# Kernel optimization log

Hardware: AMD Instinct MI355X
Metric: run time of the kernel (lower is better)

The kernel has to match this reference:

```python
import jax, jax.numpy as jnp
import numpy as np

B, N, DIM, HEADS, DEPTH, MLP = 4, 1024, 256, 4, 4, 1024
DH = DIM // HEADS
EPS = 1e-5


def _ln(x, g, b):
    mu = jnp.mean(x, axis=-1, keepdims=True)
    var = jnp.mean((x - mu) ** 2, axis=-1, keepdims=True)
    return (x - mu) / jnp.sqrt(var + EPS) * g + b


def setup_inputs() -> dict:
    key = jax.random.key(0)
    ks = jax.random.split(key, 10)
    s = 0.02
    p = {}
    p["x"] = jax.random.normal(ks[0], (B, N, DIM), jnp.float32)
    p["attn_bias"] = jax.random.normal(ks[1], (2, B, HEADS, N, N), jnp.float32)
    p["ln1_g"] = jnp.ones((DEPTH, DIM), jnp.float32)
    p["ln1_b"] = jnp.zeros((DEPTH, DIM), jnp.float32)
    p["Wkv"] = jax.random.normal(ks[2], (DEPTH, DIM, 2 * DIM), jnp.float32) * s
    p["Wq"] = jax.random.normal(ks[3], (DEPTH, DIM, DIM), jnp.float32) * s
    p["Wo"] = jax.random.normal(ks[4], (DEPTH, DIM, DIM), jnp.float32) * s
    p["bo"] = jnp.zeros((DEPTH, DIM), jnp.float32)
    p["ln2_g"] = jnp.ones((DEPTH, DIM), jnp.float32)
    p["ln2_b"] = jnp.zeros((DEPTH, DIM), jnp.float32)
    p["W1"] = jax.random.normal(ks[5], (DEPTH, DIM, MLP), jnp.float32) * s
    p["b1"] = jnp.zeros((DEPTH, MLP), jnp.float32)
    p["W2"] = jax.random.normal(ks[6], (DEPTH, MLP, DIM), jnp.float32) * s
    p["b2"] = jnp.zeros((DEPTH, DIM), jnp.float32)
    p["Wg"] = jax.random.normal(ks[7], (DIM, DIM), jnp.float32) * s
    p["lng_g"] = jnp.ones((DIM,), jnp.float32)
    p["lng_b"] = jnp.zeros((DIM,), jnp.float32)
    return p


def reference(x, attn_bias, ln1_g, ln1_b, Wkv, Wq, Wo, bo, ln2_g, ln2_b, W1, b1, W2, b2, Wg, lng_g, lng_b):
    scale = DIM ** -0.5
    add_attn = attn_bias[0] + attn_bias[1]            # [B,H,N,N]
    # aggregation bias matrices are layer-invariant (recomputed identically each layer in torch)
    A = jnp.mean(attn_bias[0], axis=1)                # [B,N,N]
    S = jnp.mean(attn_bias[1], axis=1)
    G = jax.nn.softmax(A * S, axis=2)                 # [B,N,N]

    def split_heads(t):  # [B,N,DIM] -> [B,H,N,DH]
        return t.reshape(B, N, HEADS, DH).transpose(0, 2, 1, 3)

    for l in range(DEPTH):
        # softmax-GCN aggregation
        x_ma = jax.nn.relu(_ln(jnp.matmul(G, x) @ Wg, lng_g, lng_b))
        # attention (PreNorm on x only; q comes from un-normed x_ma)
        xn = _ln(x, ln1_g[l], ln1_b[l])
        kv = xn @ Wkv[l]
        k, v = jnp.split(kv, 2, axis=-1)
        q = x_ma @ Wq[l]
        qh, kh, vh = split_heads(q), split_heads(k), split_heads(v)
        dots = jnp.einsum('bhid,bhjd->bhij', qh, kh) * scale + add_attn
        attn = jax.nn.softmax(dots, axis=-1)
        out = jnp.einsum('bhij,bhjd->bhid', attn, vh)
        out = out.transpose(0, 2, 1, 3).reshape(B, N, DIM)
        x = x + out @ Wo[l] + bo[l]
        # feed-forward (exact GELU, matching torch nn.GELU default)
        xn2 = _ln(x, ln2_g[l], ln2_b[l])
        x = x + jax.nn.gelu(xn2 @ W1[l] + b1[l], approximate=False) @ W2[l] + b2[l]
    return x
```

## Files before the change

### kernel.cpp

```cpp
#include <hip/hip_runtime.h>
#include <hip/hip_bf16.h>
#include <math.h>

typedef unsigned short u16;
typedef __bf16 bf16x8 __attribute__((ext_vector_type(8)));
typedef float f32x4 __attribute__((ext_vector_type(4)));

#define B_ 4
#define N_ 1024
#define DIM_ 256
#define HEADS_ 4
#define DH_ 64
#define MLP_ 1024
#define DEPTH_ 4

__device__ __forceinline__ float r2f(u16 r){ return __uint_as_float(((unsigned)r)<<16); }
__device__ __forceinline__ u16 f2r(float f){ __hip_bfloat16 h = __float2bfloat16(f); return *(u16*)&h; }

__device__ __forceinline__ float gelu_exact(float v){
  return 0.5f*v*(1.0f + erff(v*0.70710678118654752440f));
}

#define MFMA16(a,b,c) __builtin_amdgcn_mfma_f32_16x16x32_bf16(a,b,c,0,0,0)

__global__ void prep_bias(const float* __restrict__ bias, u16* __restrict__ G, u16* __restrict__ bsum){
  int blk = blockIdx.x;
  int i = blk & (N_-1);
  int b = blk >> 10;
  int t = threadIdx.x;
  __shared__ float red[256];
  long long base0 = ((long long)(b*HEADS_)*N_ + i)*(long long)N_;
  const long long hs = (long long)N_*N_;
  const long long cs = (long long)B_*HEADS_*N_*N_;
  int j0 = t*4;
  f32x4 a = {0.f,0.f,0.f,0.f}, s = {0.f,0.f,0.f,0.f};
  #pragma unroll
  for (int h=0;h<HEADS_;h++){
    f32x4 x0 = *(const f32x4*)(bias + base0 + h*hs + j0);
    f32x4 x1 = *(const f32x4*)(bias + cs + base0 + h*hs + j0);
    a += x0; s += x1;
    union { ushort4 u; u16 e[4]; } pk;
    #pragma unroll
    for (int k=0;k<4;k++) pk.e[k] = f2r(x0[k]+x1[k]);
    *(ushort4*)(bsum + base0 + h*hs + j0) = pk.u;
  }
  float v[4]; float lmax = -3e38f;
  #pragma unroll
  for (int k=0;k<4;k++){ v[k] = (a[k]*0.25f)*(s[k]*0.25f); lmax = fmaxf(lmax, v[k]); }
  red[t]=lmax; __syncthreads();
  for (int st=128;st>0;st>>=1){ if(t<st) red[t]=fmaxf(red[t],red[t+st]); __syncthreads(); }
  float m = red[0]; __syncthreads();
  float e[4]; float lsum = 0.f;
  #pragma unroll
  for (int k=0;k<4;k++){ e[k] = __expf(v[k]-m); lsum += e[k]; }
  red[t]=lsum; __syncthreads();
  for (int st=128;st>0;st>>=1){ if(t<st) red[t]+=red[t+st]; __syncthreads(); }
  float inv = 1.0f/red[0];
  u16* Grow = G + ((long long)b*N_ + i)*(long long)N_;
  union { ushort4 u; u16 e[4]; } pg;
  #pragma unroll
  for (int k=0;k<4;k++) pg.e[k] = f2r(e[k]*inv);
  *(ushort4*)(Grow + j0) = pg.u;
}

__global__ void ln_kernel(const float* __restrict__ X, u16* __restrict__ Y,
                          const float* __restrict__ g, const float* __restrict__ bvec){
  int row = blockIdx.x*8 + (threadIdx.x>>5);
  int cg = threadIdx.x&31;
  const float* xp = X + (long long)row*DIM_ + cg*8;
  f32x4 v0 = *(const f32x4*)xp;
  f32x4 v1 = *(const f32x4*)(xp+4);
  float s = v0[0]+v0[1]+v0[2]+v0[3]+v1[0]+v1[1]+v1[2]+v1[3];
  s += __shfl_xor(s,1); s += __shfl_xor(s,2); s += __shfl_xor(s,4); s += __shfl_xor(s,8); s += __shfl_xor(s,16);
  float mu = s*(1.0f/256.0f);
  float s2 = 0.f;
  #pragma unroll
  for (int k=0;k<4;k++){ float d=v0[k]-mu; s2 += d*d; }
  #pragma unroll
  for (int k=0;k<4;k++){ float d=v1[k]-mu; s2 += d*d; }
  s2 += __shfl_xor(s2,1); s2 += __shfl_xor(s2,2); s2 += __shfl_xor(s2,4); s2 += __shfl_xor(s2,8); s2 += __shfl_xor(s2,16);
  float rstd = rsqrtf(s2*(1.0f/256.0f)+1e-5f);
  f32x4 g0 = *(const f32x4*)(g + cg*8);
  f32x4 g1 = *(const f32x4*)(g + cg*8 + 4);
  f32x4 b0 = *(const f32x4*)(bvec + cg*8);
  f32x4 b1 = *(const f32x4*)(bvec + cg*8 + 4);
  union { ushort4 u[2]; u16 e[8]; } pk;
  #pragma unroll
  for (int k=0;k<4;k++) pk.e[k]   = f2r((v0[k]-mu)*rstd*g0[k] + b0[k]);
  #pragma unroll
  for (int k=0;k<4;k++) pk.e[4+k] = f2r((v1[k]-mu)*rstd*g1[k] + b1[k]);
  u16* yp = Y + (long long)row*DIM_ + cg*8;
  *(ushort4*)yp = pk.u[0];
  *(ushort4*)(yp+4) = pk.u[1];
}

__global__ void tcast_all(const float* __restrict__ Wkv, const float* __restrict__ Wq,
                          const float* __restrict__ Wo, const float* __restrict__ W1,
                          const float* __restrict__ W2, const float* __restrict__ Wg,
                          const float* __restrict__ xin,
                          u16* WkvT, u16* WqT, u16* WoT, u16* W1T, u16* W2T, u16* WgT, u16* xT){
  int z = blockIdx.z;
  const float* I; u16* O; int ldin, R, C;
  if (z < 4)       { I = Wkv + z*131072;      O = WkvT + z*131072;      ldin=512;  R=256;  C=512;  }
  else if (z < 8)  { I = Wq  + (z-4)*65536;   O = WqT  + (z-4)*65536;   ldin=256;  R=256;  C=256;  }
  else if (z < 12) { I = Wo  + (z-8)*65536;   O = WoT  + (z-8)*65536;   ldin=256;  R=256;  C=256;  }
  else if (z < 16) { I = W1  + (z-12)*262144; O = W1T  + (z-12)*262144; ldin=1024; R=256;  C=1024; }
  else if (z < 20) { I = W2  + (z-16)*262144; O = W2T  + (z-16)*262144; ldin=256;  R=1024; C=256;  }
  else if (z == 20){ I = Wg;                  O = WgT;                  ldin=256;  R=256;  C=256;  }
  else             { I = xin + (z-21)*262144; O = xT   + (z-21)*262144; ldin=256;  R=1024; C=256;  }
  int c0 = blockIdx.x*32, r0 = blockIdx.y*32;
  if (c0 >= C || r0 >= R) return;
  __shared__ float tile[32][33];
  int tx = threadIdx.x, ty = threadIdx.y;
  #pragma unroll
  for (int i=0;i<4;i++)
    tile[ty*4+i][tx] = I[(long long)(r0+ty*4+i)*ldin + c0+tx];
  __syncthreads();
  #pragma unroll
  for (int i=0;i<4;i++)
    O[(long long)(c0+ty*4+i)*R + r0+tx] = f2r(tile[tx][ty*4+i]);
}

__global__ __launch_bounds__(512) void layer_pre(
    const u16* __restrict__ Gb, const u16* __restrict__ xT, const u16* __restrict__ xnb,
    const u16* __restrict__ WgT, const u16* __restrict__ WqT, const u16* __restrict__ WkvT,
    const float* __restrict__ lng, const float* __restrict__ lnb,
    u16* __restrict__ qb, u16* __restrict__ kvb, u16* __restrict__ vt)
{
  __shared__ float Gx_s[16][264];
  __shared__ float t2_s[16][264];
  __shared__ u16  xma_s[16][264];
  int tid = threadIdx.x;
  int w = tid>>6, lane = tid&63, lr = lane&15, qd = lane>>4;
  int row0 = blockIdx.x*16;
  int batch = row0>>10, brow0 = row0&1023;

  {
    int kw = w>>2, cw = w&3;
    const u16* Ap = Gb + (long long)batch*1048576 + (long long)(brow0+lr)*1024 + kw*512;
    const u16* Bp = xT + (long long)batch*262144 + (long long)kw*512;
    f32x4 acc[4] = {};
    for (int k0=0;k0<512;k0+=32){
      bf16x8 af = *(const bf16x8*)(Ap + k0 + qd*8);
      #pragma unroll
      for (int nt=0;nt<4;nt++){
        bf16x8 bf = *(const bf16x8*)(Bp + (long long)(cw*64+nt*16+lr)*1024 + k0 + qd*8);
        acc[nt] = MFMA16(af,bf,acc[nt]);
      }
    }
    if (kw==0){
      #pragma unroll
      for (int nt=0;nt<4;nt++)
        #pragma unroll
        for (int r=0;r<4;r++) Gx_s[qd*4+r][cw*64+nt*16+lr] = acc[nt][r];
    }
    __syncthreads();
    if (kw==1){
      #pragma unroll
      for (int nt=0;nt<4;nt++)
        #pragma unroll
        for (int r=0;r<4;r++) Gx_s[qd*4+r][cw*64+nt*16+lr] += acc[nt][r];
    }
    __syncthreads();
  }
  {
    int r = tid>>5, cg = tid&31;
    #pragma unroll
    for (int i=0;i<8;i++) xma_s[r][cg*8+i] = f2r(Gx_s[r][cg*8+i]);
  }
  __syncthreads();
  {
    f32x4 acc[2] = {};
    for (int k0=0;k0<256;k0+=32){
      bf16x8 af = *(const bf16x8*)&xma_s[lr][k0+qd*8];
      #pragma unroll
      for (int i=0;i<2;i++){
        bf16x8 bf = *(const bf16x8*)(WgT + (long long)((w*2+i)*16+lr)*256 + k0 + qd*8);
        acc[i] = MFMA16(af,bf,acc[i]);
      }
    }
    #pragma unroll
    for (int i=0;i<2;i++)
      #pragma unroll
      for (int r=0;r<4;r++) t2_s[qd*4+r][(w*2+i)*16+lr] = acc[i][r];
  }
  __syncthreads();
  {
    int r = tid>>5, cg = tid&31;
    float v[8]; float s=0.f;
    #pragma unroll
    for (int i=0;i<8;i++){ v[i] = t2_s[r][cg*8+i]; s += v[i]; }
    s += __shfl_xor(s,1); s += __shfl_xor(s,2); s += __shfl_xor(s,4); s += __shfl_xor(s,8); s += __shfl_xor(s,16);
    float mu = s*(1.0f/256.0f);
    float s2=0.f;
    #pragma unroll
    for (int i=0;i<8;i++){ float d=v[i]-mu; s2 += d*d; }
    s2 += __shfl_xor(s2,1); s2 += __shfl_xor(s2,2); s2 += __shfl_xor(s2,4); s2 += __shfl_xor(s2,8); s2 += __shfl_xor(s2,16);
    float rstd = rsqrtf(s2*(1.0f/256.0f)+1e-5f);
    #pragma unroll
    for (int i=0;i<8;i++){
      int c = cg*8+i;
      float y = (v[i]-mu)*rstd*lng[c] + lnb[c];
      xma_s[r][c] = f2r(fmaxf(y,0.f));
    }
  }
  __syncthreads();
  {
    f32x4 acc[2] = {};
    for (int k0=0;k0<256;k0+=32){
      bf16x8 af = *(const bf16x8*)&xma_s[lr][k0+qd*8];
      #pragma unroll
      for (int i=0;i<2;i++){
        bf16x8 bf = *(const bf16x8*)(WqT + (long long)((w*2+i)*16+lr)*256 + k0 + qd*8);
        acc[i] = MFMA16(af,bf,acc[i]);
      }
    }
    #pragma unroll
    for (int i=0;i<2;i++)
      #pragma unroll
      for (int r=0;r<4;r++)
        qb[(long long)(row0+qd*4+r)*DIM_ + (w*2+i)*16+lr] = f2r(acc[i][r]);
  }
  {
    const u16* Ap = xnb + (long long)(row0+lr)*DIM_;
    f32x4 acc[4] = {};
    for (int k0=0;k0<256;k0+=32){
      bf16x8 af = *(const bf16x8*)(Ap + k0 + qd*8);
      #pragma unroll
      for (int i=0;i<4;i++){
        bf16x8 bf = *(const bf16x8*)(WkvT + (long long)((w*4+i)*16+lr)*256 + k0 + qd*8);
        acc[i] = MFMA16(af,bf,acc[i]);
      }
    }
    #pragma unroll
    for (int i=0;i<4;i++){
      int col = (w*4+i)*16+lr;
      #pragma unroll
      for (int r=0;r<4;r++){
        int row = row0+qd*4+r;
        float v = acc[i][r];
        kvb[(long long)row*512 + col] = f2r(v);
        if (col >= 256)
          vt[(long long)batch*262144 + (long long)(col-256)*1024 + (row&1023)] = f2r(v);
      }
    }
  }
}

__global__ __launch_bounds__(512) void flash_attn(
    const u16* __restrict__ qb, const u16* __restrict__ kvb,
    const u16* __restrict__ vt, const u16* __restrict__ bsum,
    u16* __restrict__ out)
{
  int z = blockIdx.z;
  int b = z>>2, h = z&3;
  int qt = blockIdx.x;
  int tid = threadIdx.x;
  int w = tid>>6, lane = tid&63;
  int g = w>>2, tw = w&3;
  int lr = lane&15, qd = lane>>4;
  __shared__ u16 Pl[8][16][72];
  __shared__ u16 sb[8][16][72];
  __shared__ float Ol[8][16][68];
  __shared__ float Ml[8][16];
  __shared__ float Ll[8][16];

  int qrow0 = qt*64 + tw*16;
  const u16* qp = qb + ((long long)(b*N_) + qrow0 + lr)*DIM_ + h*DH_;
  bf16x8 aq0 = *(const bf16x8*)(qp + qd*8);
  bf16x8 aq1 = *(const bf16x8*)(qp + 32 + qd*8);

  f32x4 oacc[4] = {};
  float m_r[4] = {-3e38f,-3e38f,-3e38f,-3e38f};
  float l_r[4] = {0.f,0.f,0.f,0.f};

  const u16* kbase = kvb + ((long long)(b*N_))*512 + h*DH_;
  const u16* vbase = vt + (long long)b*(DIM_*N_) + (long long)(h*DH_)*N_;
  const u16* bias_base = bsum + ((long long)z*N_ + qrow0)*(long long)N_;
  int srr = lane>>2, scc = (lane&3)*16;

  for (int jtl=0; jtl<8; jtl++){
    int j0 = (g*8 + jtl)*64;
    {
      const u16* gs = bias_base + (long long)srr*N_ + j0 + scc;
      uint4 t0 = *(const uint4*)gs;
      uint4 t1 = *(const uint4*)(gs+8);
      *(uint4*)&sb[w][srr][scc]   = t0;
      *(uint4*)&sb[w][srr][scc+8] = t1;
    }
    f32x4 sacc[4] = {};
    #pragma unroll
    for (int nt=0; nt<4; nt++){
      const u16* kp = kbase + (long long)(j0 + nt*16 + lr)*512;
      bf16x8 bk0 = *(const bf16x8*)(kp + qd*8);
      bf16x8 bk1 = *(const bf16x8*)(kp + 32 + qd*8);
      sacc[nt] = MFMA16(aq0, bk0, sacc[nt]);
      sacc[nt] = MFMA16(aq1, bk1, sacc[nt]);
    }
    #pragma unroll
    for (int r=0;r<4;r++){
      float pv[4];
      float vmax = -3e38f;
      #pragma unroll
      for (int nt=0;nt<4;nt++){
        float v = sacc[nt][r]*0.0625f + r2f(sb[w][qd*4+r][nt*16+lr]);
        pv[nt] = v;
        vmax = fmaxf(vmax, v);
      }
      vmax = fmaxf(vmax, __shfl_xor(vmax,1));
      vmax = fmaxf(vmax, __shfl_xor(vmax,2));
      vmax = fmaxf(vmax, __shfl_xor(vmax,4));
      vmax = fmaxf(vmax, __shfl_xor(vmax,8));
      float newm = fmaxf(m_r[r], vmax);
      float alpha = __expf(m_r[r]-newm);
      m_r[r] = newm;
      float psum = 0.f;
      #pragma unroll
      for (int nt=0;nt<4;nt++){
        float p = __expf(pv[nt]-newm);
        psum += p;
        Pl[w][qd*4+r][nt*16+lr] = f2r(p);
      }
      psum += __shfl_xor(psum,1);
      psum += __shfl_xor(psum,2);
      psum += __shfl_xor(psum,4);
      psum += __shfl_xor(psum,8);
      l_r[r] = l_r[r]*alpha + psum;
      #pragma unroll
      for (int ot=0;ot<4;ot++) oacc[ot][r] *= alpha;
    }
    #pragma unroll
    for (int ks=0;ks<2;ks++){
      bf16x8 ap = *(const bf16x8*)&Pl[w][lr][ks*32 + qd*8];
      #pragma unroll
      for (int ot=0;ot<4;ot++){
        const u16* vp = vbase + (long long)(ot*16+lr)*N_ + j0 + ks*32 + qd*8;
        bf16x8 bv = *(const bf16x8*)vp;
        oacc[ot] = MFMA16(ap, bv, oacc[ot]);
      }
    }
  }
  #pragma unroll
  for (int r=0;r<4;r++){
    int row = qd*4+r;
    #pragma unroll
    for (int ot=0;ot<4;ot++) Ol[w][row][ot*16+lr] = oacc[ot][r];
    if (lr==0){ Ml[w][row] = m_r[r]; Ll[w][row] = l_r[r]; }
  }
  __syncthreads();
  if (w < 4){
    #pragma unroll
    for (int r=0;r<4;r++){
      int row = qd*4+r;
      float m0 = Ml[w][row], m1 = Ml[w+4][row];
      float mm = fmaxf(m0,m1);
      float e0 = __expf(m0-mm), e1 = __expf(m1-mm);
      float inv = 1.0f/(Ll[w][row]*e0 + Ll[w+4][row]*e1);
      #pragma unroll
      for (int ot=0;ot<4;ot++){
        float o = Ol[w][row][ot*16+lr]*e0 + Ol[w+4][row][ot*16+lr]*e1;
        out[((long long)(b*N_) + qrow0 + row)*DIM_ + h*DH_ + ot*16 + lr] = f2r(o*inv);
      }
    }
  }
}

__global__ __launch_bounds__(512) void layer_post(
    const u16* __restrict__ aob, const float* __restrict__ resx,
    const u16* __restrict__ WoT, const float* __restrict__ bo,
    const float* __restrict__ ln2g, const float* __restrict__ ln2b,
    const u16* __restrict__ W1T, const float* __restrict__ b1,
    const u16* __restrict__ W2T, const float* __restrict__ b2,
    float* __restrict__ xf_out,
    const float* __restrict__ ln1g_next, const float* __restrict__ ln1b_next,
    u16* __restrict__ xn_out, u16* __restrict__ xT_out)
{
  __shared__ float v_s[16][264];
  __shared__ u16  xn2_s[16][264];
  __shared__ u16  h1_s[16][1048];
  __shared__ float xnew_s[16][264];
  int tid = threadIdx.x;
  int w = tid>>6, lane = tid&63, lr = lane&15, qd = lane>>4;
  int row0 = blockIdx.x*16;
  int batch = row0>>10;

  {
    const u16* Ap = aob + (long long)(row0+lr)*DIM_;
    f32x4 acc[2] = {};
    for (int k0=0;k0<256;k0+=32){
      bf16x8 af = *(const bf16x8*)(Ap + k0 + qd*8);
      #pragma unroll
      for (int i=0;i<2;i++){
        bf16x8 bf = *(const bf16x8*)(WoT + (long long)((w*2+i)*16+lr)*256 + k0 + qd*8);
        acc[i] = MFMA16(af,bf,acc[i]);
      }
    }
    #pragma unroll
    for (int i=0;i<2;i++){
      int col = (w*2+i)*16+lr;
      #pragma unroll
      for (int r=0;r<4;r++)
        v_s[qd*4+r][col] = acc[i][r] + bo[col] + resx[(long long)(row0+qd*4+r)*DIM_ + col];
    }
  }
  __syncthreads();
  {
    int r = tid>>5, cg = tid&31;
    float v[8]; float s=0.f;
    #pragma unroll
    for (int i=0;i<8;i++){ v[i] = v_s[r][cg*8+i]; s += v[i]; }
    s += __shfl_xor(s,1); s += __shfl_xor(s,2); s += __shfl_xor(s,4); s += __shfl_xor(s,8); s += __shfl_xor(s,16);
    float mu = s*(1.0f/256.0f);
    float s2=0.f;
    #pragma unroll
    for (int i=0;i<8;i++){ float d=v[i]-mu; s2 += d*d; }
    s2 += __shfl_xor(s2,1); s2 += __shfl_xor(s2,2); s2 += __shfl_xor(s2,4); s2 += __shfl_xor(s2,8); s2 += __shfl_xor(s2,16);
    float rstd = rsqrtf(s2*(1.0f/256.0f)+1e-5f);
    #pragma unroll
    for (int i=0;i<8;i++){
      int c = cg*8+i;
      xn2_s[r][c] = f2r((v[i]-mu)*rstd*ln2g[c] + ln2b[c]);
    }
  }
  __syncthreads();
  {
    f32x4 acc[8] = {};
    for (int k0=0;k0<256;k0+=32){
      bf16x8 af = *(const bf16x8*)&xn2_s[lr][k0+qd*8];
      #pragma unroll
      for (int i=0;i<8;i++){
        bf16x8 bf = *(const bf16x8*)(W1T + (long long)((w*8+i)*16+lr)*256 + k0 + qd*8);
        acc[i] = MFMA16(af,bf,acc[i]);
      }
    }
    #pragma unroll
    for (int i=0;i<8;i++){
      int col = (w*8+i)*16+lr;
      #pragma unroll
      for (int r=0;r<4;r++)
        h1_s[qd*4+r][col] = f2r(gelu_exact(acc[i][r] + b1[col]));
    }
  }
  __syncthreads();
  {
    f32x4 acc[2] = {};
    for (int k0=0;k0<1024;k0+=32){
      bf16x8 af = *(const bf16x8*)&h1_s[lr][k0+qd*8];
      #pragma unroll
      for (int i=0;i<2;i++){
        bf16x8 bf = *(const bf16x8*)(W2T + (long long)((w*2+i)*16+lr)*1024 + k0 + qd*8);
        acc[i] = MFMA16(af,bf,acc[i]);
      }
    }
    #pragma unroll
    for (int i=0;i<2;i++){
      int col = (w*2+i)*16+lr;
      #pragma unroll
      for (int r=0;r<4;r++){
        float v = acc[i][r] + b2[col] + v_s[qd*4+r][col];
        xf_out[(long long)(row0+qd*4+r)*DIM_ + col] = v;
        xnew_s[qd*4+r][col] = v;
      }
    }
  }
  if (ln1g_next){
    __syncthreads();
    int r = tid>>5, cg = tid&31;
    float v[8]; float s=0.f;
    #pragma unroll
    for (int i=0;i<8;i++){ v[i] = xnew_s[r][cg*8+i]; s += v[i]; }
    s += __shfl_xor(s,1); s += __shfl_xor(s,2); s += __shfl_xor(s,4); s += __shfl_xor(s,8); s += __shfl_xor(s,16);
    float mu = s*(1.0f/256.0f);
    float s2=0.f;
    #pragma unroll
    for (int i=0;i<8;i++){ float d=v[i]-mu; s2 += d*d; }
    s2 += __shfl_xor(s2,1); s2 += __shfl_xor(s2,2); s2 += __shfl_xor(s2,4); s2 += __shfl_xor(s2,8); s2 += __shfl_xor(s2,16);
    float rstd = rsqrtf(s2*(1.0f/256.0f)+1e-5f);
    int grow = row0 + r;
    #pragma unroll
    for (int i=0;i<8;i++){
      int c = cg*8+i;
      xn_out[(long long)grow*DIM_ + c] = f2r((v[i]-mu)*rstd*ln1g_next[c] + ln1b_next[c]);
      xT_out[(long long)batch*262144 + (long long)c*1024 + (grow&1023)] = f2r(v[i]);
    }
  }
}

extern "C" void kernel_launch(void* const* d_in, const int* in_sizes, int n_in,
                              void* d_out, int out_size, void* d_ws, size_t ws_size,
                              hipStream_t stream){
  const float* x_in   = (const float*)d_in[0];
  const float* abias  = (const float*)d_in[1];
  const float* ln1_g  = (const float*)d_in[2];
  const float* ln1_b  = (const float*)d_in[3];
  const float* Wkv    = (const float*)d_in[4];
  const float* Wq     = (const float*)d_in[5];
  const float* Wo     = (const float*)d_in[6];
  const float* bo     = (const float*)d_in[7];
  const float* ln2_g  = (const float*)d_in[8];
  const float* ln2_b  = (const float*)d_in[9];
  const float* W1     = (const float*)d_in[10];
  const float* b1     = (const float*)d_in[11];
  const float* W2     = (const float*)d_in[12];
  const float* b2     = (const float*)d_in[13];
  const float* Wg     = (const float*)d_in[14];
  const float* lng_g  = (const float*)d_in[15];
  const float* lng_b  = (const float*)d_in[16];

  char* ws = (char*)d_ws;
  float* xf   = (float*)(ws);
  u16*  Gb    = (u16*)(ws + (4ll<<20));
  u16*  bsum  = (u16*)(ws + (12ll<<20));
  u16*  kvb   = (u16*)(ws + (44ll<<20));
  u16*  vt    = (u16*)(ws + (48ll<<20));
  u16*  xT    = (u16*)(ws + (50ll<<20));
  u16*  xnb   = (u16*)(ws + (52ll<<20));
  u16*  qb    = (u16*)(ws + (54ll<<20));
  u16*  aob   = (u16*)(ws + (56ll<<20));
  u16*  WkvT  = (u16*)(ws + (58ll<<20));
  u16*  WqT   = (u16*)(ws + (59ll<<20));
  u16*  WoT   = (u16*)(ws + (59ll<<20) + (512ll<<10));
  u16*  W1T   = (u16*)(ws + (60ll<<20));
  u16*  W2T   = (u16*)(ws + (62ll<<20));
  u16*  WgT   = (u16*)(ws + (64ll<<20));

  dim3 b256(256), b512(512);

  prep_bias<<<dim3(B_*N_), b256, 0, stream>>>(abias, Gb, bsum);
  tcast_all<<<dim3(32,32,25), dim3(32,8), 0, stream>>>(Wkv,Wq,Wo,W1,W2,Wg,x_in,
                                                       WkvT,WqT,WoT,W1T,W2T,WgT,xT);
  ln_kernel<<<dim3(512), b256, 0, stream>>>(x_in, xnb, ln1_g, ln1_b);

  for (int l=0; l<DEPTH_; l++){
    const float* resx = (l==0) ? x_in : xf;
    layer_pre<<<dim3(256), b512, 0, stream>>>(Gb, xT, xnb,
        WgT, WqT + (long long)l*65536, WkvT + (long long)l*131072,
        lng_g, lng_b, qb, kvb, vt);
    flash_attn<<<dim3(16,1,B_*HEADS_), b512, 0, stream>>>(qb, kvb, vt, bsum, aob);
    if (l < DEPTH_-1){
      layer_post<<<dim3(256), b512, 0, stream>>>(aob, resx,
          WoT + (long long)l*65536, bo + l*DIM_, ln2_g + l*DIM_, ln2_b + l*DIM_,
          W1T + (long long)l*262144, b1 + l*MLP_, W2T + (long long)l*262144, b2 + l*DIM_,
          xf, ln1_g + (l+1)*DIM_, ln1_b + (l+1)*DIM_, xnb, xT);
    } else {
      layer_post<<<dim3(256), b512, 0, stream>>>(aob, resx,
          WoT + (long long)l*65536, bo + l*DIM_, ln2_g + l*DIM_, ln2_b + l*DIM_,
          W1T + (long long)l*262144, b1 + l*MLP_, W2T + (long long)l*262144, b2 + l*DIM_,
          (float*)d_out, nullptr, nullptr, nullptr, nullptr);
    }
  }
}
```

Before: 760.9 us.

## Double waves per block in layer kernels via split-K, halve flash-attn query tile

```diff
diff --git a/kernel.cpp b/kernel.cpp
--- a/kernel.cpp
+++ b/kernel.cpp
@@ -121,7 +121,7 @@
     O[(long long)(c0+ty*4+i)*R + r0+tx] = f2r(tile[tx][ty*4+i]);
 }
 
-__global__ __launch_bounds__(512) void layer_pre(
+__global__ __launch_bounds__(1024) void layer_pre(
     const u16* __restrict__ Gb, const u16* __restrict__ xT, const u16* __restrict__ xnb,
     const u16* __restrict__ WgT, const u16* __restrict__ WqT, const u16* __restrict__ WkvT,
     const float* __restrict__ lng, const float* __restrict__ lnb,
@@ -137,10 +137,10 @@
 
   {
     int kw = w>>2, cw = w&3;
-    const u16* Ap = Gb + (long long)batch*1048576 + (long long)(brow0+lr)*1024 + kw*512;
-    const u16* Bp = xT + (long long)batch*262144 + (long long)kw*512;
+    const u16* Ap = Gb + (long long)batch*1048576 + (long long)(brow0+lr)*1024 + kw*256;
+    const u16* Bp = xT + (long long)batch*262144 + (long long)kw*256;
     f32x4 acc[4] = {};
-    for (int k0=0;k0<512;k0+=32){
+    for (int k0=0;k0<256;k0+=32){
       bf16x8 af = *(const bf16x8*)(Ap + k0 + qd*8);
       #pragma unroll
       for (int nt=0;nt<4;nt++){
@@ -153,88 +153,125 @@
       for (int nt=0;nt<4;nt++)
         #pragma unroll
         for (int r=0;r<4;r++) Gx_s[qd*4+r][cw*64+nt*16+lr] = acc[nt][r];
+    } else if (kw==1){
+      #pragma unroll
+      for (int nt=0;nt<4;nt++)
+        #pragma unroll
+        for (int r=0;r<4;r++) t2_s[qd*4+r][cw*64+nt*16+lr] = acc[nt][r];
+    }
+    __syncthreads();
+    if (kw==2){
+      #pragma unroll
+      for (int nt=0;nt<4;nt++)
+        #pragma unroll
+        for (int r=0;r<4;r++) Gx_s[qd*4+r][cw*64+nt*16+lr] += acc[nt][r];
+    } else if (kw==3){
+      #pragma unroll
+      for (int nt=0;nt<4;nt++)
+        #pragma unroll
+        for (int r=0;r<4;r++) t2_s[qd*4+r][cw*64+nt*16+lr] += acc[nt][r];
+    }
+    __syncthreads();
+  }
+  {
+    int r = tid>>6, c0 = (tid&63)*4;
+    #pragma unroll
+    for (int k=0;k<4;k++) xma_s[r][c0+k] = f2r(Gx_s[r][c0+k] + t2_s[r][c0+k]);
+  }
+  __syncthreads();
+  {
+    int kw = w>>3, cw = w&7;
+    f32x4 acc[2] = {};
+    for (int k0=0;k0<128;k0+=32){
+      bf16x8 af = *(const bf16x8*)&xma_s[lr][kw*128 + k0 + qd*8];
+      #pragma unroll
+      for (int i=0;i<2;i++){
+        int cv = cw*2+i;
+        bf16x8 bf = *(const bf16x8*)(WgT + (long long)(cv*16+lr)*256 + kw*128 + k0 + qd*8);
+        acc[i] = MFMA16(af,bf,acc[i]);
+      }
+    }
+    if (kw==0){
+      #pragma unroll
+      for (int i=0;i<2;i++)
+        #pragma unroll
+        for (int r=0;r<4;r++) t2_s[qd*4+r][(cw*2+i)*16+lr] = acc[i][r];
     }
     __syncthreads();
     if (kw==1){
       #pragma unroll
-      for (int nt=0;nt<4;nt++)
-        #pragma unroll
-        for (int r=0;r<4;r++) Gx_s[qd*4+r][cw*64+nt*16+lr] += acc[nt][r];
-    }
-    __syncthreads();
-  }
-  {
-    int r = tid>>5, cg = tid&31;
-    #pragma unroll
-    for (int i=0;i<8;i++) xma_s[r][cg*8+i] = f2r(Gx_s[r][cg*8+i]);
+      for (int i=0;i<2;i++)
+        #pragma unroll
+        for (int r=0;r<4;r++) t2_s[qd*4+r][(cw*2+i)*16+lr] += acc[i][r];
+    }
+    __syncthreads();
+  }
+  {
+    int r = tid>>6, c0 = (tid&63)*4;
+    float v[4]; float s=0.f;
+    #pragma unroll
+    for (int i=0;i<4;i++){ v[i] = t2_s[r][c0+i]; s += v[i]; }
+    s += __shfl_xor(s,1); s += __shfl_xor(s,2); s += __shfl_xor(s,4);
+    s += __shfl_xor(s,8); s += __shfl_xor(s,16); s += __shfl_xor(s,32);
+    float mu = s*(1.0f/256.0f);
+    float s2=0.f;
+    #pragma unroll
+    for (int i=0;i<4;i++){ float d=v[i]-mu; s2 += d*d; }
+    s2 += __shfl_xor(s2,1); s2 += __shfl_xor(s2,2); s2 += __shfl_xor(s2,4);
+    s2 += __shfl_xor(s2,8); s2 += __shfl_xor(s2,16); s2 += __shfl_xor(s2,32);
+    float rstd = rsqrtf(s2*(1.0f/256.0f)+1e-5f);
+    #pragma unroll
+    for (int i=0;i<4;i++){
+      int c = c0+i;
+      float y = (v[i]-mu)*rstd*lng[c] + lnb[c];
+      xma_s[r][c] = f2r(fmaxf(y,0.f));
+    }
   }
   __syncthreads();
   {
+    int kw = w>>3, cw = w&7;
+    f32x4 acc[2] = {};
+    for (int k0=0;k0<128;k0+=32){
+      bf16x8 af = *(const bf16x8*)&xma_s[lr][kw*128 + k0 + qd*8];
+      #pragma unroll
+      for (int i=0;i<2;i++){
+        int cv = cw*2+i;
+        bf16x8 bf = *(const bf16x8*)(WqT + (long long)(cv*16+lr)*256 + kw*128 + k0 + qd*8);
+        acc[i] = MFMA16(af,bf,acc[i]);
+      }
+    }
+    if (kw==0){
+      #pragma unroll
+      for (int i=0;i<2;i++)
+        #pragma unroll
+        for (int r=0;r<4;r++) Gx_s[qd*4+r][(cw*2+i)*16+lr] = acc[i][r];
+    }
+    __syncthreads();
+    if (kw==1){
+      #pragma unroll
+      for (int i=0;i<2;i++){
+        int col = (cw*2+i)*16+lr;
+        #pragma unroll
+        for (int r=0;r<4;r++)
+          qb[(long long)(row0+qd*4+r)*DIM_ + col] = f2r(Gx_s[qd*4+r][col] + acc[i][r]);
+      }
+    }
+  }
+  {
+    const u16* Ap = xnb + (long long)(row0+lr)*DIM_;
     f32x4 acc[2] = {};
     for (int k0=0;k0<256;k0+=32){
-      bf16x8 af = *(const bf16x8*)&xma_s[lr][k0+qd*8];
-      #pragma unroll
-      for (int i=0;i<2;i++){
-        bf16x8 bf = *(const bf16x8*)(WgT + (long long)((w*2+i)*16+lr)*256 + k0 + qd*8);
+      bf16x8 af = *(const bf16x8*)(Ap + k0 + qd*8);
+      #pragma unroll
+      for (int i=0;i<2;i++){
+        int cv = w*2+i;
+        bf16x8 bf = *(const bf16x8*)(WkvT + (long long)(cv*16+lr)*256 + k0 + qd*8);
         acc[i] = MFMA16(af,bf,acc[i]);
       }
     }
     #pragma unroll
-    for (int i=0;i<2;i++)
-      #pragma unroll
-      for (int r=0;r<4;r++) t2_s[qd*4+r][(w*2+i)*16+lr] = acc[i][r];
-  }
-  __syncthreads();
-  {
-    int r = tid>>5, cg = tid&31;
-    float v[8]; float s=0.f;
-    #pragma unroll
-    for (int i=0;i<8;i++){ v[i] = t2_s[r][cg*8+i]; s += v[i]; }
-    s += __shfl_xor(s,1); s += __shfl_xor(s,2); s += __shfl_xor(s,4); s += __shfl_xor(s,8); s += __shfl_xor(s,16);
-    float mu = s*(1.0f/256.0f);
-    float s2=0.f;
-    #pragma unroll
-    for (int i=0;i<8;i++){ float d=v[i]-mu; s2 += d*d; }
-    s2 += __shfl_xor(s2,1); s2 += __shfl_xor(s2,2); s2 += __shfl_xor(s2,4); s2 += __shfl_xor(s2,8); s2 += __shfl_xor(s2,16);
-    float rstd = rsqrtf(s2*(1.0f/256.0f)+1e-5f);
-    #pragma unroll
-    for (int i=0;i<8;i++){
-      int c = cg*8+i;
-      float y = (v[i]-mu)*rstd*lng[c] + lnb[c];
-      xma_s[r][c] = f2r(fmaxf(y,0.f));
-    }
-  }
-  __syncthreads();
-  {
-    f32x4 acc[2] = {};
-    for (int k0=0;k0<256;k0+=32){
-      bf16x8 af = *(const bf16x8*)&xma_s[lr][k0+qd*8];
-      #pragma unroll
-      for (int i=0;i<2;i++){
-        bf16x8 bf = *(const bf16x8*)(WqT + (long long)((w*2+i)*16+lr)*256 + k0 + qd*8);
-        acc[i] = MFMA16(af,bf,acc[i]);
-      }
-    }
-    #pragma unroll
-    for (int i=0;i<2;i++)
-      #pragma unroll
-      for (int r=0;r<4;r++)
-        qb[(long long)(row0+qd*4+r)*DIM_ + (w*2+i)*16+lr] = f2r(acc[i][r]);
-  }
-  {
-    const u16* Ap = xnb + (long long)(row0+lr)*DIM_;
-    f32x4 acc[4] = {};
-    for (int k0=0;k0<256;k0+=32){
-      bf16x8 af = *(const bf16x8*)(Ap + k0 + qd*8);
-      #pragma unroll
-      for (int i=0;i<4;i++){
-        bf16x8 bf = *(const bf16x8*)(WkvT + (long long)((w*4+i)*16+lr)*256 + k0 + qd*8);
-        acc[i] = MFMA16(af,bf,acc[i]);
-      }
-    }
-    #pragma unroll
-    for (int i=0;i<4;i++){
-      int col = (w*4+i)*16+lr;
+    for (int i=0;i<2;i++){
+      int col = (w*2+i)*16+lr;
       #pragma unroll
       for (int r=0;r<4;r++){
         int row = row0+qd*4+r;
@@ -247,7 +284,7 @@
   }
 }
 
-__global__ __launch_bounds__(512) void flash_attn(
+__global__ __launch_bounds__(256) void flash_attn(
     const u16* __restrict__ qb, const u16* __restrict__ kvb,
     const u16* __restrict__ vt, const u16* __restrict__ bsum,
     u16* __restrict__ out)
@@ -257,15 +294,15 @@
   int qt = blockIdx.x;
   int tid = threadIdx.x;
   int w = tid>>6, lane = tid&63;
-  int g = w>>2, tw = w&3;
+  int tw = w&1, g = w>>1;
   int lr = lane&15, qd = lane>>4;
-  __shared__ u16 Pl[8][16][72];
-  __shared__ u16 sb[8][16][72];
-  __shared__ float Ol[8][16][68];
-  __shared__ float Ml[8][16];
-  __shared__ float Ll[8][16];
-
-  int qrow0 = qt*64 + tw*16;
+  __shared__ u16 Pl[4][16][72];
+  __shared__ u16 sb[4][16][72];
+  __shared__ float Ol[4][16][68];
+  __shared__ float Ml[4][16];
+  __shared__ float Ll[4][16];
+
+  int qrow0 = qt*32 + tw*16;
   const u16* qp = qb + ((long long)(b*N_) + qrow0 + lr)*DIM_ + h*DH_;
   bf16x8 aq0 = *(const bf16x8*)(qp + qd*8);
   bf16x8 aq1 = *(const bf16x8*)(qp + 32 + qd*8);
@@ -348,24 +385,25 @@
     if (lr==0){ Ml[w][row] = m_r[r]; Ll[w][row] = l_r[r]; }
   }
   __syncthreads();
-  if (w < 4){
+  if (w < 2){
     #pragma unroll
     for (int r=0;r<4;r++){
       int row = qd*4+r;
-      float m0 = Ml[w][row], m1 = Ml[w+4][row];
+      float m0 = Ml[w][row], m1 = Ml[w+2][row];
       float mm = fmaxf(m0,m1);
       float e0 = __expf(m0-mm), e1 = __expf(m1-mm);
-      float inv = 1.0f/(Ll[w][row]*e0 + Ll[w+4][row]*e1);
+      float inv = 1.0f/(Ll[w][row]*e0 + Ll[w+2][row]*e1);
+      int qr = qt*32 + w*16;
       #pragma unroll
       for (int ot=0;ot<4;ot++){
-        float o = Ol[w][row][ot*16+lr]*e0 + Ol[w+4][row][ot*16+lr]*e1;
-        out[((long long)(b*N_) + qrow0 + row)*DIM_ + h*DH_ + ot*16 + lr] = f2r(o*inv);
-      }
-    }
-  }
-}
-
-__global__ __launch_bounds__(512) void layer_post(
+        float o = Ol[w][row][ot*16+lr]*e0 + Ol[w+2][row][ot*16+lr]*e1;
+        out[((long long)(b*N_) + qr + row)*DIM_ + h*DH_ + ot*16 + lr] = f2r(o*inv);
+      }
+    }
+  }
+}
+
+__global__ __launch_bounds__(1024) void layer_post(
     const u16* __restrict__ aob, const float* __restrict__ resx,
     const u16* __restrict__ WoT, const float* __restrict__ bo,
     const float* __restrict__ ln2g, const float* __restrict__ ln2b,
@@ -385,57 +423,72 @@
   int batch = row0>>10;
 
   {
-    const u16* Ap = aob + (long long)(row0+lr)*DIM_;
+    int kw = w>>3, cw = w&7;
+    const u16* Ap = aob + (long long)(row0+lr)*DIM_ + kw*128;
     f32x4 acc[2] = {};
-    for (int k0=0;k0<256;k0+=32){
+    for (int k0=0;k0<128;k0+=32){
       bf16x8 af = *(const bf16x8*)(Ap + k0 + qd*8);
       #pragma unroll
       for (int i=0;i<2;i++){
-        bf16x8 bf = *(const bf16x8*)(WoT + (long long)((w*2+i)*16+lr)*256 + k0 + qd*8);
+        int cv = cw*2+i;
+        bf16x8 bf = *(const bf16x8*)(WoT + (long long)(cv*16+lr)*256 + kw*128 + k0 + qd*8);
         acc[i] = MFMA16(af,bf,acc[i]);
       }
     }
-    #pragma unroll
-    for (int i=0;i<2;i++){
-      int col = (w*2+i)*16+lr;
-      #pragma unroll
-      for (int r=0;r<4;r++)
-        v_s[qd*4+r][col] = acc[i][r] + bo[col] + resx[(long long)(row0+qd*4+r)*DIM_ + col];
-    }
-  }
-  __syncthreads();
-  {
-    int r = tid>>5, cg = tid&31;
-    float v[8]; float s=0.f;
-    #pragma unroll
-    for (int i=0;i<8;i++){ v[i] = v_s[r][cg*8+i]; s += v[i]; }
-    s += __shfl_xor(s,1); s += __shfl_xor(s,2); s += __shfl_xor(s,4); s += __shfl_xor(s,8); s += __shfl_xor(s,16);
+    if (kw==0){
+      #pragma unroll
+      for (int i=0;i<2;i++)
+        #pragma unroll
+        for (int r=0;r<4;r++) v_s[qd*4+r][(cw*2+i)*16+lr] = acc[i][r];
+    }
+    __syncthreads();
+    if (kw==1){
+      #pragma unroll
+      for (int i=0;i<2;i++){
+        int col = (cw*2+i)*16+lr;
+        #pragma unroll
+        for (int r=0;r<4;r++)
+          v_s[qd*4+r][col] = v_s[qd*4+r][col] + acc[i][r] + bo[col]
+                           + resx[(long long)(row0+qd*4+r)*DIM_ + col];
+      }
+    }
+    __syncthreads();
+  }
+  {
+    int r = tid>>6, c0 = (tid&63)*4;
+    float v[4]; float s=0.f;
+    #pragma unroll
+    for (int i=0;i<4;i++){ v[i] = v_s[r][c0+i]; s += v[i]; }
+    s += __shfl_xor(s,1); s += __shfl_xor(s,2); s += __shfl_xor(s,4);
+    s += __shfl_xor(s,8); s += __shfl_xor(s,16); s += __shfl_xor(s,32);
     float mu = s*(1.0f/256.0f);
     float s2=0.f;
     #pragma unroll
-    for (int i=0;i<8;i++){ float d=v[i]-mu; s2 += d*d; }
-    s2 += __shfl_xor(s2,1); s2 += __shfl_xor(s2,2); s2 += __shfl_xor(s2,4); s2 += __shfl_xor(s2,8); s2 += __shfl_xor(s2,16);
+    for (int i=0;i<4;i++){ float d=v[i]-mu; s2 += d*d; }
+    s2 += __shfl_xor(s2,1); s2 += __shfl_xor(s2,2); s2 += __shfl_xor(s2,4);
+    s2 += __shfl_xor(s2,8); s2 += __shfl_xor(s2,16); s2 += __shfl_xor(s2,32);
     float rstd = rsqrtf(s2*(1.0f/256.0f)+1e-5f);
     #pragma unroll
-    for (int i=0;i<8;i++){
-      int c = cg*8+i;
+    for (int i=0;i<4;i++){
+      int c = c0+i;
       xn2_s[r][c] = f2r((v[i]-mu)*rstd*ln2g[c] + ln2b[c]);
     }
   }
   __syncthreads();
   {
-    f32x4 acc[8] = {};
+    f32x4 acc[4] = {};
     for (int k0=0;k0<256;k0+=32){
       bf16x8 af = *(const bf16x8*)&xn2_s[lr][k0+qd*8];
       #pragma unroll
-      for (int i=0;i<8;i++){
-        bf16x8 bf = *(const bf16x8*)(W1T + (long long)((w*8+i)*16+lr)*256 + k0 + qd*8);
+      for (int i=0;i<4;i++){
+        int cv = w*4+i;
+        bf16x8 bf = *(const bf16x8*)(W1T + (long long)(cv*16+lr)*256 + k0 + qd*8);
         acc[i] = MFMA16(af,bf,acc[i]);
       }
     }
     #pragma unroll
-    for (int i=0;i<8;i++){
-      int col = (w*8+i)*16+lr;
+    for (int i=0;i<4;i++){
+      int col = (w*4+i)*16+lr;
       #pragma unroll
       for (int r=0;r<4;r++)
         h1_s[qd*4+r][col] = f2r(gelu_exact(acc[i][r] + b1[col]));
@@ -443,43 +496,56 @@
   }
   __syncthreads();
   {
+    int kw = w>>3, cw = w&7;
     f32x4 acc[2] = {};
-    for (int k0=0;k0<1024;k0+=32){
-      bf16x8 af = *(const bf16x8*)&h1_s[lr][k0+qd*8];
-      #pragma unroll
-      for (int i=0;i<2;i++){
-        bf16x8 bf = *(const bf16x8*)(W2T + (long long)((w*2+i)*16+lr)*1024 + k0 + qd*8);
+    for (int k0=0;k0<512;k0+=32){
+      bf16x8 af = *(const bf16x8*)&h1_s[lr][kw*512 + k0 + qd*8];
+      #pragma unroll
+      for (int i=0;i<2;i++){
+        int cv = cw*2+i;
+        bf16x8 bf = *(const bf16x8*)(W2T + (long long)(cv*16+lr)*1024 + kw*512 + k0 + qd*8);
         acc[i] = MFMA16(af,bf,acc[i]);
       }
     }
-    #pragma unroll
-    for (int i=0;i<2;i++){
-      int col = (w*2+i)*16+lr;
-      #pragma unroll
-      for (int r=0;r<4;r++){
-        float v = acc[i][r] + b2[col] + v_s[qd*4+r][col];
-        xf_out[(long long)(row0+qd*4+r)*DIM_ + col] = v;
-        xnew_s[qd*4+r][col] = v;
+    if (kw==0){
+      #pragma unroll
+      for (int i=0;i<2;i++)
+        #pragma unroll
+        for (int r=0;r<4;r++) xnew_s[qd*4+r][(cw*2+i)*16+lr] = acc[i][r];
+    }
+    __syncthreads();
+    if (kw==1){
+      #pragma unroll
+      for (int i=0;i<2;i++){
+        int col = (cw*2+i)*16+lr;
+        #pragma unroll
+        for (int r=0;r<4;r++){
+          float v = xnew_s[qd*4+r][col] + acc[i][r] + b2[col] + v_s[qd*4+r][col];
+          xf_out[(long long)(row0+qd*4+r)*DIM_ + col] = v;
+          xnew_s[qd*4+r][col] = v;
+        }
       }
     }
   }
   if (ln1g_next){
     __syncthreads();
-    int r = tid>>5, cg = tid&31;
-    float v[8]; float s=0.f;
-    #pragma unroll
-    for (int i=0;i<8;i++){ v[i] = xnew_s[r][cg*8+i]; s += v[i]; }
-    s += __shfl_xor(s,1); s += __shfl_xor(s,2); s += __shfl_xor(s,4); s += __shfl_xor(s,8); s += __shfl_xor(s,16);
+    int r = tid>>6, c0 = (tid&63)*4;
+    float v[4]; float s=0.f;
+    #pragma unroll
+    for (int i=0;i<4;i++){ v[i] = xnew_s[r][c0+i]; s += v[i]; }
+    s += __shfl_xor(s,1); s += __shfl_xor(s,2); s += __shfl_xor(s,4);
+    s += __shfl_xor(s,8); s += __shfl_xor(s,16); s += __shfl_xor(s,32);
     float mu = s*(1.0f/256.0f);
     float s2=0.f;
     #pragma unroll
-    for (int i=0;i<8;i++){ float d=v[i]-mu; s2 += d*d; }
-    s2 += __shfl_xor(s2,1); s2 += __shfl_xor(s2,2); s2 += __shfl_xor(s2,4); s2 += __shfl_xor(s2,8); s2 += __shfl_xor(s2,16);
+    for (int i=0;i<4;i++){ float d=v[i]-mu; s2 += d*d; }
+    s2 += __shfl_xor(s2,1); s2 += __shfl_xor(s2,2); s2 += __shfl_xor(s2,4);
+    s2 += __shfl_xor(s2,8); s2 += __shfl_xor(s2,16); s2 += __shfl_xor(s2,32);
     float rstd = rsqrtf(s2*(1.0f/256.0f)+1e-5f);
     int grow = row0 + r;
     #pragma unroll
-    for (int i=0;i<8;i++){
-      int c = cg*8+i;
+    for (int i=0;i<4;i++){
+      int c = c0+i;
       xn_out[(long long)grow*DIM_ + c] = f2r((v[i]-mu)*rstd*ln1g_next[c] + ln1b_next[c]);
       xT_out[(long long)batch*262144 + (long long)c*1024 + (grow&1023)] = f2r(v[i]);
     }
@@ -524,26 +590,24 @@
   u16*  W2T   = (u16*)(ws + (62ll<<20));
   u16*  WgT   = (u16*)(ws + (64ll<<20));
 
-  dim3 b256(256), b512(512);
-
-  prep_bias<<<dim3(B_*N_), b256, 0, stream>>>(abias, Gb, bsum);
+  prep_bias<<<dim3(B_*N_), dim3(256), 0, stream>>>(abias, Gb, bsum);
   tcast_all<<<dim3(32,32,25), dim3(32,8), 0, stream>>>(Wkv,Wq,Wo,W1,W2,Wg,x_in,
                                                        WkvT,WqT,WoT,W1T,W2T,WgT,xT);
-  ln_kernel<<<dim3(512), b256, 0, stream>>>(x_in, xnb, ln1_g, ln1_b);
+  ln_kernel<<<dim3(512), dim3(256), 0, stream>>>(x_in, xnb, ln1_g, ln1_b);
 
   for (int l=0; l<DEPTH_; l++){
     const float* resx = (l==0) ? x_in : xf;
-    layer_pre<<<dim3(256), b512, 0, stream>>>(Gb, xT, xnb,
+    layer_pre<<<dim3(256), dim3(1024), 0, stream>>>(Gb, xT, xnb,
         WgT, WqT + (long long)l*65536, WkvT + (long long)l*131072,
         lng_g, lng_b, qb, kvb, vt);
-    flash_attn<<<dim3(16,1,B_*HEADS_), b512, 0, stream>>>(qb, kvb, vt, bsum, aob);
+    flash_attn<<<dim3(32,1,B_*HEADS_), dim3(256), 0, stream>>>(qb, kvb, vt, bsum, aob);
     if (l < DEPTH_-1){
-      layer_post<<<dim3(256), b512, 0, stream>>>(aob, resx,
+      layer_post<<<dim3(256), dim3(1024), 0, stream>>>(aob, resx,
           WoT + (long long)l*65536, bo + l*DIM_, ln2_g + l*DIM_, ln2_b + l*DIM_,
           W1T + (long long)l*262144, b1 + l*MLP_, W2T + (long long)l*262144, b2 + l*DIM_,
           xf, ln1_g + (l+1)*DIM_, ln1_b + (l+1)*DIM_, xnb, xT);
     } else {
-      layer_post<<<dim3(256), b512, 0, stream>>>(aob, resx,
+      layer_post<<<dim3(256), dim3(1024), 0, stream>>>(aob, resx,
           WoT + (long long)l*65536, bo + l*DIM_, ln2_g + l*DIM_, ln2_b + l*DIM_,
           W1T + (long long)l*262144, b1 + l*MLP_, W2T + (long long)l*262144, b2 + l*DIM_,
           (float*)d_out, nullptr, nullptr, nullptr, nullptr);
```

Measured after the change: 784.8 us. +3.1%, slower.
